# Kernel tuning notes

Measured on AMD Instinct MI355X. Metric: run time of the kernel, lower is better.

## Reference

```python
import jax, jax.numpy as jnp
import numpy as np

DIM = 64
NUM_EXPERTS = 4
TOP_K = 2


def _dwconv3x3(x, w, b):
    # x: [B, C, H, W], w: [C, 1, 3, 3] depthwise (groups=C), b: [C]
    y = jax.lax.conv_general_dilated(
        x, w, window_strides=(1, 1), padding='SAME',
        feature_group_count=x.shape[1],
        dimension_numbers=('NCHW', 'OIHW', 'NCHW'))
    return y + b[None, :, None, None]


def setup_inputs() -> dict:
    key = jax.random.key(0)
    ks = jax.random.split(key, 12)
    B, H, W = 8, 128, 128
    s = 0.02
    return {
        'x': jax.random.normal(ks[0], (B, 2 * DIM, H, W), jnp.float32),
        'pre_w': jax.random.normal(ks[1], (DIM, 2 * DIM), jnp.float32) * s,
        'pre_b': jax.random.normal(ks[2], (DIM,), jnp.float32) * s,
        'gate_w0': jax.random.normal(ks[3], (NUM_EXPERTS, DIM), jnp.float32) * s,
        'gate_b0': jax.random.normal(ks[4], (NUM_EXPERTS,), jnp.float32) * s,
        'gate_w1': jax.random.normal(ks[5], (NUM_EXPERTS, DIM), jnp.float32) * s,
        'gate_b1': jax.random.normal(ks[6], (NUM_EXPERTS,), jnp.float32) * s,
        'exp_w1': jax.random.normal(ks[7], (NUM_EXPERTS, DIM, 1, 3, 3), jnp.float32) * s,
        'exp_b1': jax.random.normal(ks[8], (NUM_EXPERTS, DIM), jnp.float32) * s,
        'exp_w2': jax.random.normal(ks[9], (NUM_EXPERTS, DIM, 1, 3, 3), jnp.float32) * s,
        'exp_b2': jax.random.normal(ks[10], (NUM_EXPERTS, DIM), jnp.float32) * s,
    }


def reference(x, pre_w, pre_b, gate_w0, gate_b0, gate_w1, gate_b1,
              exp_w1, exp_b1, exp_w2, exp_b2):
    # pre_fuse: 1x1 conv [2*dim -> dim]
    x = jnp.einsum('bchw,oc->bohw', x, pre_w) + pre_b[None, :, None, None]

    # --- GateNetwork ---
    pooled = jnp.max(x, axis=(2, 3)) + jnp.mean(x, axis=(2, 3))  # [B, dim]
    logits = jax.nn.leaky_relu(pooled @ gate_w1.T + gate_b1, 0.2)  # [B, E]
    noise = jax.nn.softplus(pooled @ gate_w0.T + gate_b0)          # [B, E]
    n_mean = jnp.mean(noise, axis=1, keepdims=True)
    n_std = jnp.std(noise, axis=1, keepdims=True, ddof=1)          # unbiased like torch.std
    scores = logits + (noise - n_mean) / n_std
    _, topk_idx = jax.lax.top_k(scores, TOP_K)                     # [B, k]
    B = logits.shape[0]
    mask = jnp.zeros_like(logits).at[jnp.arange(B)[:, None], topk_idx].set(1.0)
    masked = jnp.where(mask > 0, logits, -jnp.inf)
    cof = jax.nn.softmax(masked, axis=1)                           # [B, E]

    # --- experts: dwconv3x3 -> GELU -> dwconv3x3, combined by gating coeffs ---
    def expert_fn(w1, b1, w2, b2):
        h = _dwconv3x3(x, w1, b1)
        h = jax.nn.gelu(h, approximate=False)
        return _dwconv3x3(h, w2, b2)

    outs = jax.vmap(expert_fn)(exp_w1, exp_b1, exp_w2, exp_b2)     # [E, B, dim, H, W]
    out = jnp.einsum('ebchw,be->bchw', outs, cof)
    return out
```

## Files before the change

### kernel.cpp

```cpp
#include <hip/hip_runtime.h>
#include <hip/hip_bf16.h>
#include <math.h>

#define HW 16384
#define IMG 128
#define C_IN 128
#define C_OUT 64
#define NB 8
#define NE 4

typedef __attribute__((ext_vector_type(8))) short bf16x8;
typedef __attribute__((ext_vector_type(4))) float f32x4;

static __device__ __forceinline__ unsigned f2bf(float f) {
  union { float f; unsigned u; } v; v.f = f;
  unsigned r = v.u + 0x7FFF + ((v.u >> 16) & 1);
  return r >> 16;
}
static __device__ __forceinline__ float bf2f_u(unsigned hbits) {
  union { unsigned u; float f; } v; v.u = hbits << 16;
  return v.f;
}
static __device__ __forceinline__ float bf2f(unsigned short h) {
  return bf2f_u((unsigned)h);
}
static __device__ __forceinline__ void pack2(float a, float b,
                                             unsigned& hi, unsigned& lo) {
  unsigned ha = f2bf(a), hb = f2bf(b);
  hi = ha | (hb << 16);
  float ra = a - bf2f_u(ha), rb = b - bf2f_u(hb);
  lo = f2bf(ra) | (f2bf(rb) << 16);
}

union FragU { unsigned u[4]; bf16x8 v; };

__global__ __launch_bounds__(64, 4) void prefuse_mfma(
    const float* __restrict__ x, const float* __restrict__ pre_w,
    const float* __restrict__ pre_b, unsigned short* __restrict__ x1,
    float* __restrict__ pmax, float* __restrict__ psum) {
  __shared__ unsigned short tbuf[16][72];
  int lane = threadIdx.x;
  int rowb = lane & 15;
  int kg = lane >> 4;
  int blk = blockIdx.x;
  int b = blk >> 9;
  int strip = blk & 511;
  int px0 = strip << 5;

  f32x4 acc[2][4];
#pragma unroll
  for (int ot = 0; ot < 4; ++ot) {
    float t = pre_b[ot * 16 + rowb];
#pragma unroll
    for (int pt = 0; pt < 2; ++pt) acc[pt][ot] = (f32x4){t, t, t, t};
  }

  for (int k = 0; k < 4; ++k) {
    bf16x8 wh[4], wl[4];
#pragma unroll
    for (int ot = 0; ot < 4; ++ot) {
      const float* wp = pre_w + (ot * 16 + rowb) * C_IN + k * 32 + kg * 8;
      float4 a = *(const float4*)wp;
      float4 c = *(const float4*)(wp + 4);
      FragU h, l;
      pack2(a.x, a.y, h.u[0], l.u[0]);
      pack2(a.z, a.w, h.u[1], l.u[1]);
      pack2(c.x, c.y, h.u[2], l.u[2]);
      pack2(c.z, c.w, h.u[3], l.u[3]);
      wh[ot] = h.v; wl[ot] = l.v;
    }
#pragma unroll
    for (int pt = 0; pt < 2; ++pt) {
      const float* ap = x + ((size_t)b * C_IN + k * 32 + kg * 8) * HW
                          + px0 + pt * 16 + rowb;
      float xv[8];
#pragma unroll
      for (int j = 0; j < 8; ++j) xv[j] = ap[(size_t)j * HW];
      FragU h, l;
      pack2(xv[0], xv[1], h.u[0], l.u[0]);
      pack2(xv[2], xv[3], h.u[1], l.u[1]);
      pack2(xv[4], xv[5], h.u[2], l.u[2]);
      pack2(xv[6], xv[7], h.u[3], l.u[3]);
#pragma unroll
      for (int ot = 0; ot < 4; ++ot) {
        acc[pt][ot] = __builtin_amdgcn_mfma_f32_16x16x32_bf16(h.v, wh[ot], acc[pt][ot], 0, 0, 0);
        acc[pt][ot] = __builtin_amdgcn_mfma_f32_16x16x32_bf16(l.v, wh[ot], acc[pt][ot], 0, 0, 0);
        acc[pt][ot] = __builtin_amdgcn_mfma_f32_16x16x32_bf16(h.v, wl[ot], acc[pt][ot], 0, 0, 0);
        acc[pt][ot] = __builtin_amdgcn_mfma_f32_16x16x32_bf16(l.v, wl[ot], acc[pt][ot], 0, 0, 0);
      }
    }
  }

#pragma unroll
  for (int ot = 0; ot < 4; ++ot) {
    float m = -INFINITY, s = 0.f;
#pragma unroll
    for (int pt = 0; pt < 2; ++pt)
#pragma unroll
      for (int r = 0; r < 4; ++r) {
        float v = acc[pt][ot][r];
        m = fmaxf(m, v); s += v;
      }
    m = fmaxf(m, __shfl_xor(m, 16)); s += __shfl_xor(s, 16);
    m = fmaxf(m, __shfl_xor(m, 32)); s += __shfl_xor(s, 32);
    if (lane < 16) {
      int idx = strip * 512 + b * 64 + ot * 16 + lane;
      pmax[idx] = m; psum[idx] = s;
    }
#pragma unroll
    for (int pt = 0; pt < 2; ++pt) {
      uint2 p;
      p.x = (f2bf(acc[pt][ot][1]) << 16) | f2bf(acc[pt][ot][0]);
      p.y = (f2bf(acc[pt][ot][3]) << 16) | f2bf(acc[pt][ot][2]);
      *(uint2*)&tbuf[rowb][pt * 16 + kg * 4] = p;
    }
    __syncthreads();
    uint4 val = *(const uint4*)&tbuf[lane >> 2][(lane & 3) * 8];
    unsigned short* op = x1 + ((size_t)b * C_OUT + ot * 16 + (lane >> 2)) * HW
                            + px0 + (lane & 3) * 8;
    *(uint4*)op = val;
    __syncthreads();
  }
}

__global__ __launch_bounds__(64) void pool2_kernel(
    const float* __restrict__ pmax, const float* __restrict__ psum,
    float* __restrict__ pooled) {
  int bo = blockIdx.x;
  int lane = threadIdx.x;
  float m = -INFINITY, s = 0.f;
#pragma unroll
  for (int i = 0; i < 8; ++i) {
    int strip = lane + (i << 6);
    m = fmaxf(m, pmax[strip * 512 + bo]);
    s += psum[strip * 512 + bo];
  }
#pragma unroll
  for (int d = 32; d >= 1; d >>= 1) {
    m = fmaxf(m, __shfl_xor(m, d));
    s += __shfl_xor(s, d);
  }
  if (lane == 0) pooled[bo] = m + s * (1.0f / HW);
}

__global__ __launch_bounds__(64) void gate_kernel(
    const float* __restrict__ pooled, const float* __restrict__ gw0,
    const float* __restrict__ gb0, const float* __restrict__ gw1,
    const float* __restrict__ gb1, float* __restrict__ cof) {
  int b = threadIdx.x;
  if (b >= NB) return;
  float logits[NE], noise[NE];
#pragma unroll
  for (int e = 0; e < NE; ++e) {
    float d0 = gb0[e], d1 = gb1[e];
    for (int k = 0; k < C_OUT; ++k) {
      float pv = pooled[b * C_OUT + k];
      d0 = fmaf(pv, gw0[e * C_OUT + k], d0);
      d1 = fmaf(pv, gw1[e * C_OUT + k], d1);
    }
    logits[e] = d1 > 0.f ? d1 : 0.2f * d1;
    noise[e] = log1pf(expf(d0));
  }
  float mn = 0.25f * (noise[0] + noise[1] + noise[2] + noise[3]);
  float var = 0.f;
#pragma unroll
  for (int e = 0; e < NE; ++e) { float d = noise[e] - mn; var += d * d; }
  float sd = sqrtf(var * (1.0f / 3.0f));
  float scores[NE];
#pragma unroll
  for (int e = 0; e < NE; ++e) scores[e] = logits[e] + (noise[e] - mn) / sd;
  int i0 = 0;
#pragma unroll
  for (int e = 1; e < NE; ++e) if (scores[e] > scores[i0]) i0 = e;
  int i1 = -1;
#pragma unroll
  for (int e = 0; e < NE; ++e)
    if (e != i0 && (i1 < 0 || scores[e] > scores[i1])) i1 = e;
  float mm = fmaxf(logits[i0], logits[i1]);
  float e0 = expf(logits[i0] - mm), e1 = expf(logits[i1] - mm);
  float inv = 1.0f / (e0 + e1);
#pragma unroll
  for (int e = 0; e < NE; ++e) cof[b * NE + e] = 0.f;
  cof[b * NE + i0] = e0 * inv;
  cof[b * NE + i1] = e1 * inv;
}

__global__ __launch_bounds__(256) void expert_kernel(
    const unsigned short* __restrict__ x1, const float* __restrict__ ew1,
    const float* __restrict__ eb1, const float* __restrict__ ew2,
    const float* __restrict__ eb2, const float* __restrict__ cof,
    float* __restrict__ out) {
  __shared__ float xs[36 * 36 + 8];
  __shared__ unsigned hs[34 * 36 + 8];
  int tid = threadIdx.x, blk = blockIdx.x;
  int tile = blk & 15, c = (blk >> 4) & 63, b = blk >> 10;
  int ty0 = (tile >> 2) * 32, tx0 = (tile & 3) * 32;
  const unsigned short* xp = x1 + ((size_t)b * C_OUT + c) * HW;

  int eA = -1, eB = -1; float cfA = 0.f, cfB = 0.f;
#pragma unroll
  for (int e = 0; e < NE; ++e) {
    float cv = cof[b * NE + e];
    if (cv != 0.f) { if (eA < 0) { eA = e; cfA = cv; } else { eB = e; cfB = cv; } }
  }
  if (eA < 0) { eA = 0; cfA = 0.f; }
  if (eB < 0) { eB = eA; cfB = 0.f; }

  float w1A[9], w1B[9], w2A[9], w2B[9];
#pragma unroll
  for (int t = 0; t < 9; ++t) {
    w1A[t] = ew1[((size_t)eA * C_OUT + c) * 9 + t];
    w1B[t] = ew1[((size_t)eB * C_OUT + c) * 9 + t];
    w2A[t] = cfA * ew2[((size_t)eA * C_OUT + c) * 9 + t];
    w2B[t] = cfB * ew2[((size_t)eB * C_OUT + c) * 9 + t];
  }
  float b1A = eb1[eA * C_OUT + c], b1B = eb1[eB * C_OUT + c];
  float bias2 = cfA * eb2[eA * C_OUT + c] + cfB * eb2[eB * C_OUT + c];

  for (int i = tid; i < 36 * 36; i += 256) {
    int iy = i / 36, ix = i - iy * 36;
    int gy = ty0 - 2 + iy, gx = tx0 - 2 + ix;
    float v = 0.f;
    if ((unsigned)gy < 128u && (unsigned)gx < 128u) v = bf2f(xp[gy * IMG + gx]);
    xs[i] = v;
  }
  __syncthreads();

  for (int t = tid; t < 34 * 9; t += 256) {
    int hr = t / 9, g4 = t - hr * 9;
    int hc0 = g4 * 4;
    const float* xr = xs + hr * 36 + hc0;
    float xv[3][6];
#pragma unroll
    for (int dy = 0; dy < 3; ++dy) {
      float4 a = *(const float4*)(xr + dy * 36);
      float2 bb = *(const float2*)(xr + dy * 36 + 4);
      xv[dy][0] = a.x; xv[dy][1] = a.y; xv[dy][2] = a.z; xv[dy][3] = a.w;
      xv[dy][4] = bb.x; xv[dy][5] = bb.y;
    }
    int gy = ty0 - 1 + hr, gx0 = tx0 - 1 + hc0;
    uint4 hv; unsigned* hp4 = (unsigned*)&hv;
#pragma unroll
    for (int j = 0; j < 4; ++j) {
      float sA = b1A, sB = b1B;
#pragma unroll
      for (int dy = 0; dy < 3; ++dy)
#pragma unroll
        for (int dx = 0; dx < 3; ++dx) {
          float xvv = xv[dy][j + dx];
          sA = fmaf(xvv, w1A[dy * 3 + dx], sA);
          sB = fmaf(xvv, w1B[dy * 3 + dx], sB);
        }
      float uA = sA * sA, uB = sB * sB;
      float tA = 1.f - uA * (0.16666667f - uA * (0.025f - uA * 0.0029761905f));
      float tB = 1.f - uB * (0.16666667f - uB * (0.025f - uB * 0.0029761905f));
      float gA = sA * fmaf(0.3989422804f * sA, tA, 0.5f);
      float gB = sB * fmaf(0.3989422804f * sB, tB, 0.5f);
      bool ok = ((unsigned)gy < 128u) && ((unsigned)(gx0 + j) < 128u);
      hp4[j] = ok ? (f2bf(gA) | (f2bf(gB) << 16)) : 0u;
    }
    *(uint4*)(hs + hr * 36 + hc0) = hv;
  }
  __syncthreads();

  int row2 = tid >> 3, oc0 = (tid & 7) * 4;
  const unsigned* hp = hs + row2 * 36 + oc0;
  float s0 = bias2, s1 = bias2, s2 = bias2, s3 = bias2;
#pragma unroll
  for (int dy = 0; dy < 3; ++dy) {
    uint4 a = *(const uint4*)(hp + dy * 36);
    uint2 bb = *(const uint2*)(hp + dy * 36 + 4);
    unsigned u[6] = {a.x, a.y, a.z, a.w, bb.x, bb.y};
    float hA[6], hB[6];
#pragma unroll
    for (int q = 0; q < 6; ++q) {
      hA[q] = bf2f_u(u[q] & 0xFFFFu);
      union { unsigned uu; float ff; } vb; vb.uu = u[q] & 0xFFFF0000u;
      hB[q] = vb.ff;
    }
    float wA0 = w2A[dy * 3], wA1 = w2A[dy * 3 + 1], wA2 = w2A[dy * 3 + 2];
    float wB0 = w2B[dy * 3], wB1 = w2B[dy * 3 + 1], wB2 = w2B[dy * 3 + 2];
    s0 = fmaf(hA[0], wA0, fmaf(hA[1], wA1, fmaf(hA[2], wA2, s0)));
    s0 = fmaf(hB[0], wB0, fmaf(hB[1], wB1, fmaf(hB[2], wB2, s0)));
    s1 = fmaf(hA[1], wA0, fmaf(hA[2], wA1, fmaf(hA[3], wA2, s1)));
    s1 = fmaf(hB[1], wB0, fmaf(hB[2], wB1, fmaf(hB[3], wB2, s1)));
    s2 = fmaf(hA[2], wA0, fmaf(hA[3], wA1, fmaf(hA[4], wA2, s2)));
    s2 = fmaf(hB[2], wB0, fmaf(hB[3], wB1, fmaf(hB[4], wB2, s2)));
    s3 = fmaf(hA[3], wA0, fmaf(hA[4], wA1, fmaf(hA[5], wA2, s3)));
    s3 = fmaf(hB[3], wB0, fmaf(hB[4], wB1, fmaf(hB[5], wB2, s3)));
  }
  float4 o4 = make_float4(s0, s1, s2, s3);
  *(float4*)(out + ((size_t)b * C_OUT + c) * HW + (ty0 + row2) * IMG + tx0 + oc0) = o4;
}

extern "C" void kernel_launch(void* const* d_in, const int* in_sizes, int n_in,
                              void* d_out, int out_size, void* d_ws, size_t ws_size,
                              hipStream_t stream) {
  const float* x     = (const float*)d_in[0];
  const float* pre_w = (const float*)d_in[1];
  const float* pre_b = (const float*)d_in[2];
  const float* gw0   = (const float*)d_in[3];
  const float* gb0   = (const float*)d_in[4];
  const float* gw1   = (const float*)d_in[5];
  const float* gb1   = (const float*)d_in[6];
  const float* ew1   = (const float*)d_in[7];
  const float* eb1   = (const float*)d_in[8];
  const float* ew2   = (const float*)d_in[9];
  const float* eb2   = (const float*)d_in[10];
  float* out = (float*)d_out;

  char* ws = (char*)d_ws;
  unsigned short* x1 = (unsigned short*)ws;
  float* pmax   = (float*)(ws + 16777216);
  float* psum   = (float*)(ws + 17825792);
  float* pooled = (float*)(ws + 18874368);
  float* cof    = (float*)(ws + 18876416);

  prefuse_mfma<<<4096, 64, 0, stream>>>(x, pre_w, pre_b, x1, pmax, psum);
  pool2_kernel<<<512, 64, 0, stream>>>(pmax, psum, pooled);
  gate_kernel<<<1, 64, 0, stream>>>(pooled, gw0, gb0, gw1, gb1, cof);
  expert_kernel<<<8192, 256, 0, stream>>>(x1, ew1, eb1, ew2, eb2, cof, out);
}
```

Measured before the change: 76.78 us.

## Precompute split-bf16 weight fragments, drop lo*lo MFMA, use hardware bf16 pack

Adds a one-block kernel that converts the pre-fuse weights into hi/lo bf16 MFMA fragments once, so the 4096 prefuse blocks load ready-made fragments instead of re-splitting the fp32 weights each time. Drops the low*low MFMA term in the split-bf16 product, cutting MFMA work by a quarter at a small cost in accuracy. Replaces the software round-to-nearest bf16 conversion with the packed hardware conversion intrinsic in all kernels. Adds one extra tiny kernel launch and a small workspace region.

```diff
diff --git a/kernel.cpp b/kernel.cpp
--- a/kernel.cpp
+++ b/kernel.cpp
@@ -12,11 +12,6 @@
 typedef __attribute__((ext_vector_type(8))) short bf16x8;
 typedef __attribute__((ext_vector_type(4))) float f32x4;
 
-static __device__ __forceinline__ unsigned f2bf(float f) {
-  union { float f; unsigned u; } v; v.f = f;
-  unsigned r = v.u + 0x7FFF + ((v.u >> 16) & 1);
-  return r >> 16;
-}
 static __device__ __forceinline__ float bf2f_u(unsigned hbits) {
   union { unsigned u; float f; } v; v.u = hbits << 16;
   return v.f;
@@ -24,20 +19,46 @@
 static __device__ __forceinline__ float bf2f(unsigned short h) {
   return bf2f_u((unsigned)h);
 }
-static __device__ __forceinline__ void pack2(float a, float b,
-                                             unsigned& hi, unsigned& lo) {
-  unsigned ha = f2bf(a), hb = f2bf(b);
-  hi = ha | (hb << 16);
-  float ra = a - bf2f_u(ha), rb = b - bf2f_u(hb);
-  lo = f2bf(ra) | (f2bf(rb) << 16);
-}
-
-union FragU { unsigned u[4]; bf16x8 v; };
+static __device__ __forceinline__ unsigned cvtpk(float a, float b) {
+  __hip_bfloat162 p = __float22bfloat162_rn(make_float2(a, b));
+  union { __hip_bfloat162 h; unsigned u; } v; v.h = p;
+  return v.u;
+}
+static __device__ __forceinline__ void pk2(float a, float b,
+                                           unsigned& hi, unsigned& lo) {
+  hi = cvtpk(a, b);
+  float ra = a - bf2f_u(hi & 0xFFFFu);
+  float rb = b - bf2f_u(hi >> 16);
+  lo = cvtpk(ra, rb);
+}
+
+union FragU { unsigned u[4]; uint4 q; bf16x8 v; };
+
+__global__ __launch_bounds__(64) void wfrag_kernel(
+    const float* __restrict__ pre_w, uint4* __restrict__ whi,
+    uint4* __restrict__ wlo) {
+  int lane = threadIdx.x;
+  int rowb = lane & 15, kg = lane >> 4;
+  for (int q = 0; q < 16; ++q) {
+    int k = q >> 2, ot = q & 3;
+    const float* wp = pre_w + (ot * 16 + rowb) * C_IN + k * 32 + kg * 8;
+    float4 a = *(const float4*)wp;
+    float4 c = *(const float4*)(wp + 4);
+    uint4 h, l;
+    pk2(a.x, a.y, h.x, l.x);
+    pk2(a.z, a.w, h.y, l.y);
+    pk2(c.x, c.y, h.z, l.z);
+    pk2(c.z, c.w, h.w, l.w);
+    whi[q * 64 + lane] = h;
+    wlo[q * 64 + lane] = l;
+  }
+}
 
 __global__ __launch_bounds__(64, 4) void prefuse_mfma(
-    const float* __restrict__ x, const float* __restrict__ pre_w,
-    const float* __restrict__ pre_b, unsigned short* __restrict__ x1,
-    float* __restrict__ pmax, float* __restrict__ psum) {
+    const float* __restrict__ x, const uint4* __restrict__ whi,
+    const uint4* __restrict__ wlo, const float* __restrict__ pre_b,
+    unsigned short* __restrict__ x1, float* __restrict__ pmax,
+    float* __restrict__ psum) {
   __shared__ unsigned short tbuf[16][72];
   int lane = threadIdx.x;
   int rowb = lane & 15;
@@ -56,18 +77,11 @@
   }
 
   for (int k = 0; k < 4; ++k) {
-    bf16x8 wh[4], wl[4];
+    FragU wh[4], wl[4];
 #pragma unroll
     for (int ot = 0; ot < 4; ++ot) {
-      const float* wp = pre_w + (ot * 16 + rowb) * C_IN + k * 32 + kg * 8;
-      float4 a = *(const float4*)wp;
-      float4 c = *(const float4*)(wp + 4);
-      FragU h, l;
-      pack2(a.x, a.y, h.u[0], l.u[0]);
-      pack2(a.z, a.w, h.u[1], l.u[1]);
-      pack2(c.x, c.y, h.u[2], l.u[2]);
-      pack2(c.z, c.w, h.u[3], l.u[3]);
-      wh[ot] = h.v; wl[ot] = l.v;
+      wh[ot].q = whi[(k * 4 + ot) * 64 + lane];
+      wl[ot].q = wlo[(k * 4 + ot) * 64 + lane];
     }
 #pragma unroll
     for (int pt = 0; pt < 2; ++pt) {
@@ -77,16 +91,15 @@
 #pragma unroll
       for (int j = 0; j < 8; ++j) xv[j] = ap[(size_t)j * HW];
       FragU h, l;
-      pack2(xv[0], xv[1], h.u[0], l.u[0]);
-      pack2(xv[2], xv[3], h.u[1], l.u[1]);
-      pack2(xv[4], xv[5], h.u[2], l.u[2]);
-      pack2(xv[6], xv[7], h.u[3], l.u[3]);
+      pk2(xv[0], xv[1], h.u[0], l.u[0]);
+      pk2(xv[2], xv[3], h.u[1], l.u[1]);
+      pk2(xv[4], xv[5], h.u[2], l.u[2]);
+      pk2(xv[6], xv[7], h.u[3], l.u[3]);
 #pragma unroll
       for (int ot = 0; ot < 4; ++ot) {
-        acc[pt][ot] = __builtin_amdgcn_mfma_f32_16x16x32_bf16(h.v, wh[ot], acc[pt][ot], 0, 0, 0);
-        acc[pt][ot] = __builtin_amdgcn_mfma_f32_16x16x32_bf16(l.v, wh[ot], acc[pt][ot], 0, 0, 0);
-        acc[pt][ot] = __builtin_amdgcn_mfma_f32_16x16x32_bf16(h.v, wl[ot], acc[pt][ot], 0, 0, 0);
-        acc[pt][ot] = __builtin_amdgcn_mfma_f32_16x16x32_bf16(l.v, wl[ot], acc[pt][ot], 0, 0, 0);
+        acc[pt][ot] = __builtin_amdgcn_mfma_f32_16x16x32_bf16(h.v, wh[ot].v, acc[pt][ot], 0, 0, 0);
+        acc[pt][ot] = __builtin_amdgcn_mfma_f32_16x16x32_bf16(l.v, wh[ot].v, acc[pt][ot], 0, 0, 0);
+        acc[pt][ot] = __builtin_amdgcn_mfma_f32_16x16x32_bf16(h.v, wl[ot].v, acc[pt][ot], 0, 0, 0);
       }
     }
   }
@@ -110,8 +123,8 @@
 #pragma unroll
     for (int pt = 0; pt < 2; ++pt) {
       uint2 p;
-      p.x = (f2bf(acc[pt][ot][1]) << 16) | f2bf(acc[pt][ot][0]);
-      p.y = (f2bf(acc[pt][ot][3]) << 16) | f2bf(acc[pt][ot][2]);
+      p.x = cvtpk(acc[pt][ot][0], acc[pt][ot][1]);
+      p.y = cvtpk(acc[pt][ot][2], acc[pt][ot][3]);
       *(uint2*)&tbuf[rowb][pt * 16 + kg * 4] = p;
     }
     __syncthreads();
@@ -257,7 +270,7 @@
       float gA = sA * fmaf(0.3989422804f * sA, tA, 0.5f);
       float gB = sB * fmaf(0.3989422804f * sB, tB, 0.5f);
       bool ok = ((unsigned)gy < 128u) && ((unsigned)(gx0 + j) < 128u);
-      hp4[j] = ok ? (f2bf(gA) | (f2bf(gB) << 16)) : 0u;
+      hp4[j] = ok ? cvtpk(gA, gB) : 0u;
     }
     *(uint4*)(hs + hr * 36 + hc0) = hv;
   }
@@ -315,8 +328,11 @@
   float* psum   = (float*)(ws + 17825792);
   float* pooled = (float*)(ws + 18874368);
   float* cof    = (float*)(ws + 18876416);
-
-  prefuse_mfma<<<4096, 64, 0, stream>>>(x, pre_w, pre_b, x1, pmax, psum);
+  uint4* whi    = (uint4*)(ws + 18878464);
+  uint4* wlo    = (uint4*)(ws + 18894848);
+
+  wfrag_kernel<<<1, 64, 0, stream>>>(pre_w, whi, wlo);
+  prefuse_mfma<<<4096, 64, 0, stream>>>(x, whi, wlo, pre_b, x1, pmax, psum);
   pool2_kernel<<<512, 64, 0, stream>>>(pmax, psum, pooled);
   gate_kernel<<<1, 64, 0, stream>>>(pooled, gw0, gb0, gw1, gb1, cof);
   expert_kernel<<<8192, 256, 0, stream>>>(x1, ew1, eb1, ew2, eb2, cof, out);
```

Result: no change. 77.63 us (+1.1%).
